# Performance work log

Hardware: AMD Instinct MI355X
Metric: run time of the kernel (lower is better)

## Reference

```python
import jax, jax.numpy as jnp
import numpy as np

VOCAB = 32000; D_MODEL = 768; N_LAYERS = 4
D_STATE = 16; D_CONV = 4; EXPAND = 2
D_INNER = EXPAND * D_MODEL                 # 1536
DT_RANK = (D_MODEL + 15) // 16             # 48
BATCH = 2; SEQ = 1024


def setup_inputs():
    key = jax.random.key(0)
    ks = jax.random.split(key, 10)
    def nrm(k, shape, scale=0.02):
        return (jax.random.normal(k, shape) * scale).astype(jnp.float32)
    inp = {}
    inp['tokens'] = jax.random.randint(ks[0], (BATCH, SEQ), 0, VOCAB)
    inp['embedding'] = nrm(ks[1], (VOCAB, D_MODEL))
    inp['head_bias'] = jnp.zeros((VOCAB,), jnp.float32)
    inp['ln_g'] = jnp.ones((N_LAYERS, D_MODEL), jnp.float32)
    inp['ln_b'] = jnp.zeros((N_LAYERS, D_MODEL), jnp.float32)
    inp['W_in'] = nrm(ks[2], (N_LAYERS, 2 * D_INNER, D_MODEL))
    inp['conv_w'] = nrm(ks[3], (N_LAYERS, D_INNER, 1, D_CONV), 0.1)
    inp['conv_b'] = jnp.zeros((N_LAYERS, D_INNER), jnp.float32)
    inp['W_xproj'] = nrm(ks[4], (N_LAYERS, DT_RANK + 2 * D_STATE, D_INNER))
    inp['W_dt'] = nrm(ks[5], (N_LAYERS, D_INNER, DT_RANK), 0.1)
    inp['b_dt'] = nrm(ks[6], (N_LAYERS, D_INNER), 0.5)
    # S4D-real init: A_n = n for n in 1..d_state
    inp['A_log'] = jnp.broadcast_to(jnp.log(jnp.arange(1, D_STATE + 1, dtype=jnp.float32)), (N_LAYERS, D_INNER, D_STATE)).copy()
    inp['D_ssm'] = jnp.ones((N_LAYERS, D_INNER), jnp.float32)
    inp['W_out'] = nrm(ks[7], (N_LAYERS, D_MODEL, D_INNER))
    inp['norm_g'] = jnp.ones((D_MODEL,), jnp.float32)
    inp['norm_b'] = jnp.zeros((D_MODEL,), jnp.float32)
    return inp


def _ln(x, g, b):
    m = jnp.mean(x, axis=-1, keepdims=True)
    v = jnp.var(x, axis=-1, keepdims=True)
    return (x - m) * jax.lax.rsqrt(v + 1e-5) * g + b


def _mamba(x, W_in, conv_w, conv_b, W_xproj, W_dt, b_dt, A_log, D_ssm, W_out):
    # x: (S, B, D_MODEL)
    xz = jnp.einsum('sbd,ed->sbe', x, W_in)           # (S, B, 2*D_INNER)
    xc, z = jnp.split(xz, 2, axis=-1)
    # depthwise causal conv along sequence
    xt = jnp.transpose(xc, (1, 2, 0))                  # (B, C, S)
    xt = jax.lax.conv_general_dilated(xt, conv_w, (1,), [(D_CONV - 1, 0)],
                                      dimension_numbers=('NCH', 'OIH', 'NCH'),
                                      feature_group_count=D_INNER)
    xt = xt + conv_b[None, :, None]
    xc = jax.nn.silu(jnp.transpose(xt, (2, 0, 1)))     # (S, B, C)
    xdb = jnp.einsum('sbc,ec->sbe', xc, W_xproj)       # (S, B, DT_RANK+2N)
    dt_r = xdb[..., :DT_RANK]
    Bm = xdb[..., DT_RANK:DT_RANK + D_STATE]
    Cm = xdb[..., DT_RANK + D_STATE:]
    dt = jax.nn.softplus(jnp.einsum('sbr,cr->sbc', dt_r, W_dt) + b_dt)
    A = -jnp.exp(A_log)                                # (C, N)

    def step(h, t):
        dt_t, B_t, C_t, x_t = t                        # (B,C),(B,N),(B,N),(B,C)
        dA = jnp.exp(dt_t[..., None] * A)              # (B, C, N)
        h = h * dA + (dt_t * x_t)[..., None] * B_t[:, None, :]
        y = jnp.einsum('bcn,bn->bc', h, C_t)
        return h, y

    h0 = jnp.zeros((x.shape[1], D_INNER, D_STATE), x.dtype)
    _, ys = jax.lax.scan(step, h0, (dt, Bm, Cm, xc))   # ys: (S, B, C)
    y = (ys + D_ssm * xc) * jax.nn.silu(z)
    return jnp.einsum('sbc,dc->sbd', y, W_out)


def reference(tokens, embedding, head_bias, ln_g, ln_b, W_in, conv_w, conv_b, W_xproj, W_dt, b_dt, A_log, D_ssm, W_out, norm_g, norm_b):
    x = embedding[tokens.T]                            # (S, B, D)
    for i in range(N_LAYERS):
        x = x + _mamba(_ln(x, ln_g[i], ln_b[i]), W_in[i], conv_w[i], conv_b[i],
                       W_xproj[i], W_dt[i], b_dt[i], A_log[i], D_ssm[i], W_out[i])
    x = _ln(x, norm_g, norm_b)
    logits = jnp.einsum('sbd,vd->sbv', x, embedding) + head_bias  # tied head
    return jnp.transpose(logits, (1, 0, 2))            # (B, S, VOCAB)
```

## Files before the change

### kernel.cpp

```cpp
#include <hip/hip_runtime.h>
#include <hip/hip_bf16.h>
#include <cstdint>
#include <cstddef>

#define SEQ_LEN 1024
#define NBATCH  2
#define MROWS   2048
#define DMODEL  768
#define DINNER  1536
#define DTRANK  48
#define DSTATE  16
#define NLAYERS 4
#define NVOCAB  32000
#define XPROJ_N 80
#define NCHUNK  16
#define CHUNK   64
#define GROUPS  (NBATCH * DINNER)
#define SCANW   (GROUPS * DSTATE)
#define XSPLIT  8

typedef __attribute__((ext_vector_type(4))) float f32x4;
typedef __attribute__((ext_vector_type(8))) short s16x8;
using bf16 = __hip_bfloat16;

__device__ __forceinline__ float b2f(bf16 v){ return __bfloat162float(v); }
__device__ __forceinline__ bf16  f2b(float v){ return __float2bfloat16(v); }
__device__ __forceinline__ short f2bs(float v){
  return (short)__builtin_bit_cast(unsigned short, __float2bfloat16(v));
}

__device__ __forceinline__ void glds16(const ushort* g, ushort* l) {
  __builtin_amdgcn_global_load_lds(
      (const __attribute__((address_space(1))) void*)g,
      (__attribute__((address_space(3))) void*)l,
      16, 0, 0);
}

#define CVT_E0 6144000
#define CVT_E1 (CVT_E0 + 2359296)
#define CVT_E2 (CVT_E1 + 1179648)
#define CVT_E3 (CVT_E2 + 122880)
#define CVT_E4 (CVT_E3 + 73728)
__global__ __launch_bounds__(256) void k_cvt5(
    const float* __restrict__ s0, const float* __restrict__ s1,
    const float* __restrict__ s2, const float* __restrict__ s3,
    const float* __restrict__ s4,
    ushort* __restrict__ d0, ushort* __restrict__ d1,
    ushort* __restrict__ d2, ushort* __restrict__ d3,
    ushort* __restrict__ d4)
{
  int i = blockIdx.x * 256 + threadIdx.x;
  const float* s; ushort* d; int base;
  if      (i < CVT_E0) { s = s0; d = d0; base = 0; }
  else if (i < CVT_E1) { s = s1; d = d1; base = CVT_E0; }
  else if (i < CVT_E2) { s = s2; d = d2; base = CVT_E1; }
  else if (i < CVT_E3) { s = s3; d = d3; base = CVT_E2; }
  else if (i < CVT_E4) { s = s4; d = d4; base = CVT_E3; }
  else return;
  int li = i - base;
  f32x4 v = *(const f32x4*)(s + (size_t)li * 4);
  ushort4 o;
  o.x = (ushort)f2bs(v[0]); o.y = (ushort)f2bs(v[1]);
  o.z = (ushort)f2bs(v[2]); o.w = (ushort)f2bs(v[3]);
  *(ushort4*)(d + (size_t)li * 4) = o;
}

__global__ __launch_bounds__(256) void k_xsum(const float* __restrict__ p,
    ushort* __restrict__ out, int n4) {
  int i = blockIdx.x * 256 + threadIdx.x;
  if (i >= n4) return;
  f32x4 s = {};
#pragma unroll
  for (int z = 0; z < XSPLIT; z++) {
    f32x4 v = *(const f32x4*)(p + (size_t)z * (MROWS * XPROJ_N) + (size_t)i * 4);
    s[0] += v[0]; s[1] += v[1]; s[2] += v[2]; s[3] += v[3];
  }
  ushort4 o;
  o.x = (ushort)f2bs(s[0]); o.y = (ushort)f2bs(s[1]);
  o.z = (ushort)f2bs(s[2]); o.w = (ushort)f2bs(s[3]);
  *(ushort4*)(out + (size_t)i * 4) = o;
}

__device__ __forceinline__ void ln_rows(const float v0[3], int t,
    const float* __restrict__ g, const float* __restrict__ b,
    bf16* __restrict__ outrow) {
  float s = 0.f, s2 = 0.f;
#pragma unroll
  for (int j = 0; j < 3; j++) { s += v0[j]; s2 += v0[j] * v0[j]; }
#pragma unroll
  for (int o = 32; o >= 1; o >>= 1) { s += __shfl_xor(s, o); s2 += __shfl_xor(s2, o); }
  __shared__ float red[8];
  int wave = t >> 6;
  if ((t & 63) == 0) { red[wave] = s; red[4 + wave] = s2; }
  __syncthreads();
  s  = red[0] + red[1] + red[2] + red[3];
  s2 = red[4] + red[5] + red[6] + red[7];
  float mean = s * (1.f / DMODEL);
  float var  = s2 * (1.f / DMODEL) - mean * mean;
  float rstd = rsqrtf(var + 1e-5f);
#pragma unroll
  for (int j = 0; j < 3; j++) {
    int d = t + j * 256;
    outrow[d] = f2b((v0[j] - mean) * rstd * g[d] + b[d]);
  }
}

__global__ __launch_bounds__(256) void k_ln(const float* __restrict__ x,
    bf16* __restrict__ out, const float* __restrict__ g, const float* __restrict__ b) {
  int m = blockIdx.x;
  const float* row = x + (size_t)m * DMODEL;
  int t = threadIdx.x;
  float v0[3];
#pragma unroll
  for (int j = 0; j < 3; j++) v0[j] = row[t + j * 256];
  ln_rows(v0, t, g, b, out + (size_t)m * DMODEL);
}

__global__ __launch_bounds__(256) void k_embed_ln(const int* __restrict__ tok,
    const float* __restrict__ emb, float* __restrict__ x,
    bf16* __restrict__ out, const float* __restrict__ g, const float* __restrict__ b) {
  int m = blockIdx.x;
  const float* row = emb + (size_t)tok[m] * DMODEL;
  int t = threadIdx.x;
  float v0[3];
#pragma unroll
  for (int j = 0; j < 3; j++) {
    v0[j] = row[t + j * 256];
    x[(size_t)m * DMODEL + t + j * 256] = v0[j];
  }
  ln_rows(v0, t, g, b, out + (size_t)m * DMODEL);
}

template<bool HAS_BIAS, int OMODE>
__global__ __launch_bounds__(256) void k_gemm128(
    const ushort* __restrict__ A, int lda,
    const ushort* __restrict__ B, int ldb,
    void* __restrict__ C, int ldc,
    const float* __restrict__ bias,
    int M, int N, int K)
{
  __shared__ ushort As[2][128 * 32];
  __shared__ ushort Bs[2][128 * 32];
  const int t = threadIdx.x;
  const int lane = t & 63;
  const int wave = t >> 6;
  const int tile_m = blockIdx.x * 128;
  const int tile_n = blockIdx.y * 128;
  const int kper = K / gridDim.z;
  const int kb = blockIdx.z * kper;
  const int ke = kb + kper;
  const int wr = (wave >> 1) * 64;
  const int wc = (wave & 1) * 64;

  f32x4 acc[4][4] = {};

  const int sr = wave * 32 + (lane >> 2);
  const int sc = (lane & 3) * 8;
  const ushort* gA0 = A + (size_t)(tile_m + sr) * lda + sc + kb;
  const ushort* gA1 = gA0 + (size_t)16 * lda;
  const ushort* gB0 = B + (size_t)(tile_n + sr) * ldb + sc + kb;
  const ushort* gB1 = gB0 + (size_t)16 * ldb;

  const int fr = lane & 15;
  const int kk = (lane >> 4) * 8;

  auto stage = [&](int bb) {
    glds16(gA0, &As[bb][wave * 1024]);
    glds16(gA1, &As[bb][wave * 1024 + 512]);
    glds16(gB0, &Bs[bb][wave * 1024]);
    glds16(gB1, &Bs[bb][wave * 1024 + 512]);
    gA0 += 32; gA1 += 32; gB0 += 32; gB1 += 32;
  };

  stage(0);
  int cur = 0;

  for (int k0 = kb; k0 < ke; k0 += 32) {
    if (k0 + 32 < ke) {
      stage(cur ^ 1);
      asm volatile("s_waitcnt vmcnt(4)" ::: "memory");
    } else {
      asm volatile("s_waitcnt vmcnt(0)" ::: "memory");
    }
    __builtin_amdgcn_s_barrier();

    s16x8 a[4], b[4];
#pragma unroll
    for (int m = 0; m < 4; m++)
      a[m] = *(const s16x8*)&As[cur][(wr + m * 16 + fr) * 32 + kk];
#pragma unroll
    for (int n = 0; n < 4; n++)
      b[n] = *(const s16x8*)&Bs[cur][(wc + n * 16 + fr) * 32 + kk];
#pragma unroll
    for (int m = 0; m < 4; m++)
#pragma unroll
      for (int n = 0; n < 4; n++)
        acc[m][n] = __builtin_amdgcn_mfma_f32_16x16x32_bf16(a[m], b[n], acc[m][n], 0, 0, 0);

    __builtin_amdgcn_s_barrier();
    cur ^= 1;
  }

  const int rq = (lane >> 4) * 4;
#pragma unroll
  for (int m = 0; m < 4; m++)
#pragma unroll
    for (int n = 0; n < 4; n++) {
      int colg = tile_n + wc + n * 16 + fr;
      float bv = HAS_BIAS ? bias[colg] : 0.f;
#pragma unroll
      for (int r = 0; r < 4; r++) {
        int rowg = tile_m + wr + m * 16 + rq + r;
        size_t idx = (size_t)rowg * ldc + colg;
        float v = acc[m][n][r] + bv;
        if constexpr (OMODE == 0) ((float*)C)[idx] = v;
        else if constexpr (OMODE == 1) atomicAdd((float*)C + idx, v);
        else ((bf16*)C)[idx] = f2b(v);
      }
    }
}

template<bool HAS_BIAS>
__global__ __launch_bounds__(512) void k_gemm256(
    const ushort* __restrict__ A, int lda,
    const ushort* __restrict__ B, int ldb,
    float* __restrict__ C, int ldc,
    const float* __restrict__ bias,
    int M, int N, int K)
{
  __shared__ ushort As[2][256 * 32];
  __shared__ ushort Bs[2][256 * 32];
  const int t = threadIdx.x;
  const int lane = t & 63;
  const int wave = t >> 6;
  const int tile_m = blockIdx.x * 256;
  const int tile_n = blockIdx.y * 256;
  const int wr = (wave >> 2) * 128;
  const int wc = (wave & 3) * 64;

  f32x4 acc[8][4] = {};

  const int sr = wave * 16 + (lane >> 2);
  const int sc = (lane & 3) * 8;
  const ushort* gA0 = A + (size_t)(tile_m + sr) * lda + sc;
  const ushort* gA1 = A + (size_t)(tile_m + 128 + sr) * lda + sc;
  const ushort* gB0 = B + (size_t)(tile_n + sr) * ldb + sc;
  const ushort* gB1 = B + (size_t)(tile_n + 128 + sr) * ldb + sc;

  const int fr = lane & 15;
  const int kk = (lane >> 4) * 8;

  auto stage = [&](int bb) {
    glds16(gA0, &As[bb][wave * 512]);
    glds16(gA1, &As[bb][4096 + wave * 512]);
    glds16(gB0, &Bs[bb][wave * 512]);
    glds16(gB1, &Bs[bb][4096 + wave * 512]);
    gA0 += 32; gA1 += 32; gB0 += 32; gB1 += 32;
  };

  stage(0);
  int cur = 0;

  for (int k0 = 0; k0 < K; k0 += 32) {
    if (k0 + 32 < K) {
      stage(cur ^ 1);
      asm volatile("s_waitcnt vmcnt(4)" ::: "memory");
    } else {
      asm volatile("s_waitcnt vmcnt(0)" ::: "memory");
    }
    __builtin_amdgcn_s_barrier();

    s16x8 a[8], b[4];
#pragma unroll
    for (int m = 0; m < 8; m++)
      a[m] = *(const s16x8*)&As[cur][(wr + m * 16 + fr) * 32 + kk];
#pragma unroll
    for (int n = 0; n < 4; n++)
      b[n] = *(const s16x8*)&Bs[cur][(wc + n * 16 + fr) * 32 + kk];
#pragma unroll
    for (int m = 0; m < 8; m++)
#pragma unroll
      for (int n = 0; n < 4; n++)
        acc[m][n] = __builtin_amdgcn_mfma_f32_16x16x32_bf16(a[m], b[n], acc[m][n], 0, 0, 0);

    __builtin_amdgcn_s_barrier();
    cur ^= 1;
  }

  const int rq = (lane >> 4) * 4;
#pragma unroll
  for (int m = 0; m < 8; m++)
#pragma unroll
    for (int n = 0; n < 4; n++) {
      int colg = tile_n + wc + n * 16 + fr;
      float bv = HAS_BIAS ? bias[colg] : 0.f;
#pragma unroll
      for (int r = 0; r < 4; r++) {
        int rowg = tile_m + wr + m * 16 + rq + r;
        __builtin_nontemporal_store(acc[m][n][r] + bv, &C[(size_t)rowg * ldc + colg]);
      }
    }
}

template<int MODE>
__global__ __launch_bounds__(256) void k_gemm(
    const ushort* __restrict__ A, int lda,
    const ushort* __restrict__ W, int ldw,
    void* __restrict__ Cout, int ldc,
    int M, int N, int K,
    const float* __restrict__ bias,
    const float* __restrict__ xcp,
    float* __restrict__ dtxp)
{
  __shared__ ushort As[64][40];
  __shared__ ushort Ws[64][40];
  const int tile_m = blockIdx.x * 64;
  const int tile_n = blockIdx.y * 64;
  const int t = threadIdx.x;
  const int lane = t & 63;
  const int wave = t >> 6;
  const int wr = (wave >> 1) * 32;
  const int wc = (wave & 1) * 32;
  f32x4 acc[2][2] = {};

  const int kper = ((K + gridDim.z - 1) / gridDim.z + 31) & ~31;
  const int kb = blockIdx.z * kper;
  int ke = kb + kper; if (ke > K) ke = K;

  const int srow = t >> 2;
  const int scol = (t & 3) * 8;

  for (int k0 = kb; k0 < ke; k0 += 32) {
    {
      int gm = tile_m + srow, gk = k0 + scol;
      s16x8 v = {};
      if (gm < M) {
        if (gk + 8 <= K) v = *(const s16x8*)(A + (size_t)gm * lda + gk);
        else {
#pragma unroll
          for (int j = 0; j < 8; j++) if (gk + j < K) v[j] = (short)A[(size_t)gm * lda + gk + j];
        }
      }
      *(s16x8*)&As[srow][scol] = v;
    }
    {
      int gn = tile_n + srow, gk = k0 + scol;
      s16x8 v = {};
      if (gn < N) {
        if (gk + 8 <= K) v = *(const s16x8*)(W + (size_t)gn * ldw + gk);
        else {
#pragma unroll
          for (int j = 0; j < 8; j++) if (gk + j < K) v[j] = (short)W[(size_t)gn * ldw + gk + j];
        }
      }
      *(s16x8*)&Ws[srow][scol] = v;
    }
    __syncthreads();
    const int kk = (lane >> 4) * 8;
    const int fr = lane & 15;
    s16x8 a0 = *(const s16x8*)&As[wr + fr][kk];
    s16x8 a1 = *(const s16x8*)&As[wr + 16 + fr][kk];
    s16x8 b0 = *(const s16x8*)&Ws[wc + fr][kk];
    s16x8 b1 = *(const s16x8*)&Ws[wc + 16 + fr][kk];
    acc[0][0] = __builtin_amdgcn_mfma_f32_16x16x32_bf16(a0, b0, acc[0][0], 0, 0, 0);
    acc[0][1] = __builtin_amdgcn_mfma_f32_16x16x32_bf16(a0, b1, acc[0][1], 0, 0, 0);
    acc[1][0] = __builtin_amdgcn_mfma_f32_16x16x32_bf16(a1, b0, acc[1][0], 0, 0, 0);
    acc[1][1] = __builtin_amdgcn_mfma_f32_16x16x32_bf16(a1, b1, acc[1][1], 0, 0, 0);
    __syncthreads();
  }

  const int fr = lane & 15;
  const int rq = (lane >> 4) * 4;
#pragma unroll
  for (int i = 0; i < 2; i++)
#pragma unroll
    for (int j = 0; j < 2; j++) {
      int colg = tile_n + wc + j * 16 + fr;
#pragma unroll
      for (int r = 0; r < 4; r++) {
        int rowg = tile_m + wr + i * 16 + rq + r;
        if (rowg < M && colg < N) {
          float v = acc[i][j][r];
          size_t idx = (size_t)rowg * ldc + colg;
          if constexpr (MODE == 0) {
            ((bf16*)Cout)[idx] = f2b(v);
          } else if constexpr (MODE == 2) {
            v += bias[colg];
            float sp = (v > 20.f) ? v : log1pf(__expf(v));
            ((float*)Cout)[idx] = sp;
            dtxp[idx] = sp * xcp[idx];
          } else {
            ((float*)Cout)[(size_t)blockIdx.z * (MROWS * XPROJ_N) + idx] = v;
          }
        }
      }
    }
}

__global__ __launch_bounds__(256) void k_conv(const bf16* __restrict__ xz,
    const float* __restrict__ w, const float* __restrict__ cb,
    float* __restrict__ xc, bf16* __restrict__ xcb) {
  int id = blockIdx.x * 256 + threadIdx.x;
  int m = id / DINNER, c = id - m * DINNER;
  int s = m & (SEQ_LEN - 1);
  float acc = cb[c];
#pragma unroll
  for (int k = 0; k < 4; k++) {
    int sp = s - 3 + k;
    if (sp >= 0) acc += w[c * 4 + k] * b2f(xz[(size_t)(m - 3 + k) * (2 * DINNER) + c]);
  }
  float sil = acc / (1.f + __expf(-acc));
  xc[id] = sil;
  xcb[id] = f2b(sil);
}

__global__ __launch_bounds__(256) void k_scan1(const float* __restrict__ dt,
    const float* __restrict__ dtx, const bf16* __restrict__ xdb,
    const float* __restrict__ A_log, float* __restrict__ aprod,
    float* __restrict__ hend) {
  int gid = blockIdx.x * 256 + threadIdx.x;
  int n  = gid & 15;
  int t2 = gid >> 4;
  int j  = t2 / GROUPS;
  int cb = t2 - j * GROUPS;
  int c  = cb % DINNER;
  int b  = cb / DINNER;
  float Acn = -__expf(A_log[c * DSTATE + n]);
  float h = 0.f, ap = 1.f;
  int mbase = b * SEQ_LEN + j * CHUNK;
#pragma unroll 4
  for (int s = 0; s < CHUNK; s++) {
    int m = mbase + s;
    float dtv = dt[(size_t)m * DINNER + c];
    float dxv = dtx[(size_t)m * DINNER + c];
    float Bv  = b2f(xdb[(size_t)m * XPROJ_N + DTRANK + n]);
    float dA  = __expf(dtv * Acn);
    h = h * dA + dxv * Bv;
    ap *= dA;
  }
  aprod[gid] = ap;
  hend[gid]  = h;
}

__global__ __launch_bounds__(256) void k_scan2(const float* __restrict__ aprod,
    const float* __restrict__ hend, float* __restrict__ hin) {
  int idx = blockIdx.x * 256 + threadIdx.x;
  float h = 0.f;
#pragma unroll
  for (int j = 0; j < NCHUNK; j++) {
    hin[(size_t)j * SCANW + idx] = h;
    h = aprod[(size_t)j * SCANW + idx] * h + hend[(size_t)j * SCANW + idx];
  }
}

__global__ __launch_bounds__(256) void k_scan3(const float* __restrict__ dt,
    const float* __restrict__ dtx, const bf16* __restrict__ xdb,
    const float* __restrict__ A_log, const float* __restrict__ hin,
    float* __restrict__ y) {
  int gid = blockIdx.x * 256 + threadIdx.x;
  int n  = gid & 15;
  int t2 = gid >> 4;
  int j  = t2 / GROUPS;
  int cb = t2 - j * GROUPS;
  int c  = cb % DINNER;
  int b  = cb / DINNER;
  float Acn = -__expf(A_log[c * DSTATE + n]);
  float h = hin[gid];
  int mbase = b * SEQ_LEN + j * CHUNK;
#pragma unroll 2
  for (int s = 0; s < CHUNK; s++) {
    int m = mbase + s;
    float dtv = dt[(size_t)m * DINNER + c];
    float dxv = dtx[(size_t)m * DINNER + c];
    float Bv  = b2f(xdb[(size_t)m * XPROJ_N + DTRANK + n]);
    float Cv  = b2f(xdb[(size_t)m * XPROJ_N + DTRANK + DSTATE + n]);
    float dA  = __expf(dtv * Acn);
    h = h * dA + dxv * Bv;
    float p = h * Cv;
    p += __shfl_xor(p, 8);
    p += __shfl_xor(p, 4);
    p += __shfl_xor(p, 2);
    p += __shfl_xor(p, 1);
    if (n == 0) y[(size_t)m * DINNER + c] = p;
  }
}

__global__ __launch_bounds__(256) void k_ycomb(const float* __restrict__ y,
    const float* __restrict__ xc, const bf16* __restrict__ xz,
    const float* __restrict__ D_ssm, bf16* __restrict__ ybf) {
  int id = blockIdx.x * 256 + threadIdx.x;
  int m = id / DINNER, c = id - m * DINNER;
  float z = b2f(xz[(size_t)m * (2 * DINNER) + DINNER + c]);
  float sil = z / (1.f + __expf(-z));
  float v = (y[id] + D_ssm[c] * xc[id]) * sil;
  ybf[id] = f2b(v);
}

extern "C" void kernel_launch(void* const* d_in, const int* in_sizes, int n_in,
                              void* d_out, int out_size, void* d_ws, size_t ws_size,
                              hipStream_t stream) {
  const int*   tokens    = (const int*)  d_in[0];
  const float* embedding = (const float*)d_in[1];
  const float* head_bias = (const float*)d_in[2];
  const float* ln_g      = (const float*)d_in[3];
  const float* ln_b      = (const float*)d_in[4];
  const float* W_in      = (const float*)d_in[5];
  const float* conv_w    = (const float*)d_in[6];
  const float* conv_b    = (const float*)d_in[7];
  const float* W_xproj   = (const float*)d_in[8];
  const float* W_dt      = (const float*)d_in[9];
  const float* b_dt      = (const float*)d_in[10];
  const float* A_log     = (const float*)d_in[11];
  const float* D_ssm     = (const float*)d_in[12];
  const float* W_out     = (const float*)d_in[13];
  const float* norm_g    = (const float*)d_in[14];
  const float* norm_b    = (const float*)d_in[15];
  float* out = (float*)d_out;

  char* ws = (char*)d_ws;
  size_t off = 0;
  auto alloc = [&](size_t bytes) -> char* {
    char* p = ws + off;
    off = (off + bytes + 255) & ~(size_t)255;
    return p;
  };
  float*  x     = (float*) alloc((size_t)MROWS * DMODEL * 4);
  bf16*   xln   = (bf16*)  alloc((size_t)MROWS * DMODEL * 2);
  bf16*   xz    = (bf16*)  alloc((size_t)MROWS * 2 * DINNER * 2);
  float*  xc    = (float*) alloc((size_t)MROWS * DINNER * 4);
  bf16*   xcb   = (bf16*)  alloc((size_t)MROWS * DINNER * 2);
  bf16*   xdb   = (bf16*)  alloc((size_t)MROWS * XPROJ_N * 2);
  float*  xdbp  = (float*) alloc((size_t)XSPLIT * MROWS * XPROJ_N * 4);
  float*  dtf   = (float*) alloc((size_t)MROWS * DINNER * 4);
  float*  dtx   = (float*) alloc((size_t)MROWS * DINNER * 4);
  float*  yraw  = (float*) alloc((size_t)MROWS * DINNER * 4);
  bf16*   ybf   = (bf16*)  alloc((size_t)MROWS * DINNER * 2);
  float*  aprod = (float*) alloc((size_t)SCANW * NCHUNK * 4);
  float*  hend  = (float*) alloc((size_t)SCANW * NCHUNK * 4);
  float*  hin   = (float*) alloc((size_t)SCANW * NCHUNK * 4);
  ushort* ebf   = (ushort*)alloc((size_t)NVOCAB * DMODEL * 2);
  ushort* winb  = (ushort*)alloc((size_t)NLAYERS * 2 * DINNER * DMODEL * 2);
  ushort* wxpb  = (ushort*)alloc((size_t)NLAYERS * XPROJ_N * DINNER * 2);
  ushort* wdtb  = (ushort*)alloc((size_t)NLAYERS * DINNER * DTRANK * 2);
  ushort* woutb = (ushort*)alloc((size_t)NLAYERS * DMODEL * DINNER * 2);
  (void)ws_size; (void)in_sizes; (void)n_in; (void)out_size;

  k_cvt5<<<(CVT_E4 + 255) / 256, 256, 0, stream>>>(
      embedding, W_in, W_out, W_xproj, W_dt,
      ebf, winb, woutb, wxpb, wdtb);

  k_embed_ln<<<MROWS, 256, 0, stream>>>(tokens, embedding, x, xln, ln_g, ln_b);

  const int XDBN4 = MROWS * XPROJ_N / 4;

  for (int L = 0; L < NLAYERS; L++) {
    if (L > 0)
      k_ln<<<MROWS, 256, 0, stream>>>(x, xln, ln_g + L * DMODEL, ln_b + L * DMODEL);

    k_gemm128<false, 2><<<dim3(MROWS / 128, (2 * DINNER) / 128), 256, 0, stream>>>(
        (const ushort*)xln, DMODEL,
        winb + (size_t)L * 2 * DINNER * DMODEL, DMODEL,
        (void*)xz, 2 * DINNER, nullptr, MROWS, 2 * DINNER, DMODEL);

    k_conv<<<MROWS * DINNER / 256, 256, 0, stream>>>(
        xz, conv_w + (size_t)L * DINNER * 4, conv_b + (size_t)L * DINNER, xc, xcb);

    k_gemm<3><<<dim3(MROWS / 64, 2, XSPLIT), 256, 0, stream>>>(
        (const ushort*)xcb, DINNER,
        wxpb + (size_t)L * XPROJ_N * DINNER, DINNER,
        (void*)xdbp, XPROJ_N, MROWS, XPROJ_N, DINNER,
        nullptr, nullptr, nullptr);
    k_xsum<<<(XDBN4 + 255) / 256, 256, 0, stream>>>(xdbp, (ushort*)xdb, XDBN4);

    k_gemm<2><<<dim3(MROWS / 64, DINNER / 64), 256, 0, stream>>>(
        (const ushort*)xdb, XPROJ_N,
        wdtb + (size_t)L * DINNER * DTRANK, DTRANK,
        (void*)dtf, DINNER, MROWS, DINNER, DTRANK,
        b_dt + (size_t)L * DINNER, xc, dtx);

    const float* Al = A_log + (size_t)L * DINNER * DSTATE;
    k_scan1<<<SCANW * NCHUNK / 256, 256, 0, stream>>>(dtf, dtx, xdb, Al, aprod, hend);
    k_scan2<<<SCANW / 256, 256, 0, stream>>>(aprod, hend, hin);
    k_scan3<<<SCANW * NCHUNK / 256, 256, 0, stream>>>(dtf, dtx, xdb, Al, hin, yraw);

    k_ycomb<<<MROWS * DINNER / 256, 256, 0, stream>>>(
        yraw, xc, xz, D_ssm + (size_t)L * DINNER, ybf);

    k_gemm128<false, 1><<<dim3(MROWS / 128, DMODEL / 128, 4), 256, 0, stream>>>(
        (const ushort*)ybf, DINNER,
        woutb + (size_t)L * DMODEL * DINNER, DINNER,
        (void*)x, DMODEL, nullptr, MROWS, DMODEL, DINNER);
  }

  k_ln<<<MROWS, 256, 0, stream>>>(x, xln, norm_g, norm_b);

  k_gemm256<true><<<dim3(MROWS / 256, NVOCAB / 256), 512, 0, stream>>>(
      (const ushort*)xln, DMODEL,
      ebf, DMODEL,
      out, NVOCAB, head_bias, MROWS, NVOCAB, DMODEL);
}
```

Before: 989.2 us.

## Store SSM intermediates in bf16 and use 8-wave 128x128 GEMM everywhere

Drops the fp32 copy of the conv output and stores dt*x and the scan output y as bf16 instead of fp32, to cut memory traffic in the conv, scan and combine kernels. The 128x128 GEMM moves from 4 to 8 waves, each wave owning a 32x64 sub-tile, for more latency hiding. The 256x256 head GEMM is removed and the vocab projection now uses the 128-tile kernel. This gives up some operand reuse in the large head GEMM and loses some precision in the scan inputs and outputs.

Result: no change. 980.9 us (-0.8%).

```diff
diff --git a/kernel.cpp b/kernel.cpp
--- a/kernel.cpp
+++ b/kernel.cpp
@@ -132,7 +132,7 @@
 }
 
 template<bool HAS_BIAS, int OMODE>
-__global__ __launch_bounds__(256) void k_gemm128(
+__global__ __launch_bounds__(512, 4) void k_gemm128(
     const ushort* __restrict__ A, int lda,
     const ushort* __restrict__ B, int ldb,
     void* __restrict__ C, int ldc,
@@ -149,27 +149,23 @@
   const int kper = K / gridDim.z;
   const int kb = blockIdx.z * kper;
   const int ke = kb + kper;
-  const int wr = (wave >> 1) * 64;
+  const int wr = (wave >> 1) * 32;
   const int wc = (wave & 1) * 64;
 
-  f32x4 acc[4][4] = {};
-
-  const int sr = wave * 32 + (lane >> 2);
+  f32x4 acc[2][4] = {};
+
+  const int sr = wave * 16 + (lane >> 2);
   const int sc = (lane & 3) * 8;
-  const ushort* gA0 = A + (size_t)(tile_m + sr) * lda + sc + kb;
-  const ushort* gA1 = gA0 + (size_t)16 * lda;
-  const ushort* gB0 = B + (size_t)(tile_n + sr) * ldb + sc + kb;
-  const ushort* gB1 = gB0 + (size_t)16 * ldb;
+  const ushort* gA = A + (size_t)(tile_m + sr) * lda + sc + kb;
+  const ushort* gB = B + (size_t)(tile_n + sr) * ldb + sc + kb;
 
   const int fr = lane & 15;
   const int kk = (lane >> 4) * 8;
 
   auto stage = [&](int bb) {
-    glds16(gA0, &As[bb][wave * 1024]);
-    glds16(gA1, &As[bb][wave * 1024 + 512]);
-    glds16(gB0, &Bs[bb][wave * 1024]);
-    glds16(gB1, &Bs[bb][wave * 1024 + 512]);
-    gA0 += 32; gA1 += 32; gB0 += 32; gB1 += 32;
+    glds16(gA, &As[bb][wave * 512]);
+    glds16(gB, &Bs[bb][wave * 512]);
+    gA += 32; gB += 32;
   };
 
   stage(0);
@@ -178,21 +174,21 @@
   for (int k0 = kb; k0 < ke; k0 += 32) {
     if (k0 + 32 < ke) {
       stage(cur ^ 1);
-      asm volatile("s_waitcnt vmcnt(4)" ::: "memory");
+      asm volatile("s_waitcnt vmcnt(2)" ::: "memory");
     } else {
       asm volatile("s_waitcnt vmcnt(0)" ::: "memory");
     }
     __builtin_amdgcn_s_barrier();
 
-    s16x8 a[4], b[4];
-#pragma unroll
-    for (int m = 0; m < 4; m++)
+    s16x8 a[2], b[4];
+#pragma unroll
+    for (int m = 0; m < 2; m++)
       a[m] = *(const s16x8*)&As[cur][(wr + m * 16 + fr) * 32 + kk];
 #pragma unroll
     for (int n = 0; n < 4; n++)
       b[n] = *(const s16x8*)&Bs[cur][(wc + n * 16 + fr) * 32 + kk];
 #pragma unroll
-    for (int m = 0; m < 4; m++)
+    for (int m = 0; m < 2; m++)
 #pragma unroll
       for (int n = 0; n < 4; n++)
         acc[m][n] = __builtin_amdgcn_mfma_f32_16x16x32_bf16(a[m], b[n], acc[m][n], 0, 0, 0);
@@ -203,7 +199,7 @@
 
   const int rq = (lane >> 4) * 4;
 #pragma unroll
-  for (int m = 0; m < 4; m++)
+  for (int m = 0; m < 2; m++)
 #pragma unroll
     for (int n = 0; n < 4; n++) {
       int colg = tile_n + wc + n * 16 + fr;
@@ -220,88 +216,6 @@
     }
 }
 
-template<bool HAS_BIAS>
-__global__ __launch_bounds__(512) void k_gemm256(
-    const ushort* __restrict__ A, int lda,
-    const ushort* __restrict__ B, int ldb,
-    float* __restrict__ C, int ldc,
-    const float* __restrict__ bias,
-    int M, int N, int K)
-{
-  __shared__ ushort As[2][256 * 32];
-  __shared__ ushort Bs[2][256 * 32];
-  const int t = threadIdx.x;
-  const int lane = t & 63;
-  const int wave = t >> 6;
-  const int tile_m = blockIdx.x * 256;
-  const int tile_n = blockIdx.y * 256;
-  const int wr = (wave >> 2) * 128;
-  const int wc = (wave & 3) * 64;
-
-  f32x4 acc[8][4] = {};
-
-  const int sr = wave * 16 + (lane >> 2);
-  const int sc = (lane & 3) * 8;
-  const ushort* gA0 = A + (size_t)(tile_m + sr) * lda + sc;
-  const ushort* gA1 = A + (size_t)(tile_m + 128 + sr) * lda + sc;
-  const ushort* gB0 = B + (size_t)(tile_n + sr) * ldb + sc;
-  const ushort* gB1 = B + (size_t)(tile_n + 128 + sr) * ldb + sc;
-
-  const int fr = lane & 15;
-  const int kk = (lane >> 4) * 8;
-
-  auto stage = [&](int bb) {
-    glds16(gA0, &As[bb][wave * 512]);
-    glds16(gA1, &As[bb][4096 + wave * 512]);
-    glds16(gB0, &Bs[bb][wave * 512]);
-    glds16(gB1, &Bs[bb][4096 + wave * 512]);
-    gA0 += 32; gA1 += 32; gB0 += 32; gB1 += 32;
-  };
-
-  stage(0);
-  int cur = 0;
-
-  for (int k0 = 0; k0 < K; k0 += 32) {
-    if (k0 + 32 < K) {
-      stage(cur ^ 1);
-      asm volatile("s_waitcnt vmcnt(4)" ::: "memory");
-    } else {
-      asm volatile("s_waitcnt vmcnt(0)" ::: "memory");
-    }
-    __builtin_amdgcn_s_barrier();
-
-    s16x8 a[8], b[4];
-#pragma unroll
-    for (int m = 0; m < 8; m++)
-      a[m] = *(const s16x8*)&As[cur][(wr + m * 16 + fr) * 32 + kk];
-#pragma unroll
-    for (int n = 0; n < 4; n++)
-      b[n] = *(const s16x8*)&Bs[cur][(wc + n * 16 + fr) * 32 + kk];
-#pragma unroll
-    for (int m = 0; m < 8; m++)
-#pragma unroll
-      for (int n = 0; n < 4; n++)
-        acc[m][n] = __builtin_amdgcn_mfma_f32_16x16x32_bf16(a[m], b[n], acc[m][n], 0, 0, 0);
-
-    __builtin_amdgcn_s_barrier();
-    cur ^= 1;
-  }
-
-  const int rq = (lane >> 4) * 4;
-#pragma unroll
-  for (int m = 0; m < 8; m++)
-#pragma unroll
-    for (int n = 0; n < 4; n++) {
-      int colg = tile_n + wc + n * 16 + fr;
-      float bv = HAS_BIAS ? bias[colg] : 0.f;
-#pragma unroll
-      for (int r = 0; r < 4; r++) {
-        int rowg = tile_m + wr + m * 16 + rq + r;
-        __builtin_nontemporal_store(acc[m][n][r] + bv, &C[(size_t)rowg * ldc + colg]);
-      }
-    }
-}
-
 template<int MODE>
 __global__ __launch_bounds__(256) void k_gemm(
     const ushort* __restrict__ A, int lda,
@@ -309,8 +223,8 @@
     void* __restrict__ Cout, int ldc,
     int M, int N, int K,
     const float* __restrict__ bias,
-    const float* __restrict__ xcp,
-    float* __restrict__ dtxp)
+    const bf16* __restrict__ xcb,
+    bf16* __restrict__ dtxp)
 {
   __shared__ ushort As[64][40];
   __shared__ ushort Ws[64][40];
@@ -388,7 +302,7 @@
             v += bias[colg];
             float sp = (v > 20.f) ? v : log1pf(__expf(v));
             ((float*)Cout)[idx] = sp;
-            dtxp[idx] = sp * xcp[idx];
+            dtxp[idx] = f2b(sp * b2f(xcb[idx]));
           } else {
             ((float*)Cout)[(size_t)blockIdx.z * (MROWS * XPROJ_N) + idx] = v;
           }
@@ -399,7 +313,7 @@
 
 __global__ __launch_bounds__(256) void k_conv(const bf16* __restrict__ xz,
     const float* __restrict__ w, const float* __restrict__ cb,
-    float* __restrict__ xc, bf16* __restrict__ xcb) {
+    bf16* __restrict__ xcb) {
   int id = blockIdx.x * 256 + threadIdx.x;
   int m = id / DINNER, c = id - m * DINNER;
   int s = m & (SEQ_LEN - 1);
@@ -410,12 +324,11 @@
     if (sp >= 0) acc += w[c * 4 + k] * b2f(xz[(size_t)(m - 3 + k) * (2 * DINNER) + c]);
   }
   float sil = acc / (1.f + __expf(-acc));
-  xc[id] = sil;
   xcb[id] = f2b(sil);
 }
 
 __global__ __launch_bounds__(256) void k_scan1(const float* __restrict__ dt,
-    const float* __restrict__ dtx, const bf16* __restrict__ xdb,
+    const bf16* __restrict__ dtx, const bf16* __restrict__ xdb,
     const float* __restrict__ A_log, float* __restrict__ aprod,
     float* __restrict__ hend) {
   int gid = blockIdx.x * 256 + threadIdx.x;
@@ -432,7 +345,7 @@
   for (int s = 0; s < CHUNK; s++) {
     int m = mbase + s;
     float dtv = dt[(size_t)m * DINNER + c];
-    float dxv = dtx[(size_t)m * DINNER + c];
+    float dxv = b2f(dtx[(size_t)m * DINNER + c]);
     float Bv  = b2f(xdb[(size_t)m * XPROJ_N + DTRANK + n]);
     float dA  = __expf(dtv * Acn);
     h = h * dA + dxv * Bv;
@@ -454,9 +367,9 @@
 }
 
 __global__ __launch_bounds__(256) void k_scan3(const float* __restrict__ dt,
-    const float* __restrict__ dtx, const bf16* __restrict__ xdb,
+    const bf16* __restrict__ dtx, const bf16* __restrict__ xdb,
     const float* __restrict__ A_log, const float* __restrict__ hin,
-    float* __restrict__ y) {
+    bf16* __restrict__ y) {
   int gid = blockIdx.x * 256 + threadIdx.x;
   int n  = gid & 15;
   int t2 = gid >> 4;
@@ -471,7 +384,7 @@
   for (int s = 0; s < CHUNK; s++) {
     int m = mbase + s;
     float dtv = dt[(size_t)m * DINNER + c];
-    float dxv = dtx[(size_t)m * DINNER + c];
+    float dxv = b2f(dtx[(size_t)m * DINNER + c]);
     float Bv  = b2f(xdb[(size_t)m * XPROJ_N + DTRANK + n]);
     float Cv  = b2f(xdb[(size_t)m * XPROJ_N + DTRANK + DSTATE + n]);
     float dA  = __expf(dtv * Acn);
@@ -481,18 +394,18 @@
     p += __shfl_xor(p, 4);
     p += __shfl_xor(p, 2);
     p += __shfl_xor(p, 1);
-    if (n == 0) y[(size_t)m * DINNER + c] = p;
-  }
-}
-
-__global__ __launch_bounds__(256) void k_ycomb(const float* __restrict__ y,
-    const float* __restrict__ xc, const bf16* __restrict__ xz,
+    if (n == 0) y[(size_t)m * DINNER + c] = f2b(p);
+  }
+}
+
+__global__ __launch_bounds__(256) void k_ycomb(const bf16* __restrict__ y,
+    const bf16* __restrict__ xcb, const bf16* __restrict__ xz,
     const float* __restrict__ D_ssm, bf16* __restrict__ ybf) {
   int id = blockIdx.x * 256 + threadIdx.x;
   int m = id / DINNER, c = id - m * DINNER;
   float z = b2f(xz[(size_t)m * (2 * DINNER) + DINNER + c]);
   float sil = z / (1.f + __expf(-z));
-  float v = (y[id] + D_ssm[c] * xc[id]) * sil;
+  float v = (b2f(y[id]) + D_ssm[c] * b2f(xcb[id])) * sil;
   ybf[id] = f2b(v);
 }
 
@@ -527,13 +440,12 @@
   float*  x     = (float*) alloc((size_t)MROWS * DMODEL * 4);
   bf16*   xln   = (bf16*)  alloc((size_t)MROWS * DMODEL * 2);
   bf16*   xz    = (bf16*)  alloc((size_t)MROWS * 2 * DINNER * 2);
-  float*  xc    = (float*) alloc((size_t)MROWS * DINNER * 4);
   bf16*   xcb   = (bf16*)  alloc((size_t)MROWS * DINNER * 2);
   bf16*   xdb   = (bf16*)  alloc((size_t)MROWS * XPROJ_N * 2);
   float*  xdbp  = (float*) alloc((size_t)XSPLIT * MROWS * XPROJ_N * 4);
   float*  dtf   = (float*) alloc((size_t)MROWS * DINNER * 4);
-  float*  dtx   = (float*) alloc((size_t)MROWS * DINNER * 4);
-  float*  yraw  = (float*) alloc((size_t)MROWS * DINNER * 4);
+  bf16*   dtx   = (bf16*)  alloc((size_t)MROWS * DINNER * 2);
+  bf16*   yraw  = (bf16*)  alloc((size_t)MROWS * DINNER * 2);
   bf16*   ybf   = (bf16*)  alloc((size_t)MROWS * DINNER * 2);
   float*  aprod = (float*) alloc((size_t)SCANW * NCHUNK * 4);
   float*  hend  = (float*) alloc((size_t)SCANW * NCHUNK * 4);
@@ -557,13 +469,13 @@
     if (L > 0)
       k_ln<<<MROWS, 256, 0, stream>>>(x, xln, ln_g + L * DMODEL, ln_b + L * DMODEL);
 
-    k_gemm128<false, 2><<<dim3(MROWS / 128, (2 * DINNER) / 128), 256, 0, stream>>>(
+    k_gemm128<false, 2><<<dim3(MROWS / 128, (2 * DINNER) / 128), 512, 0, stream>>>(
         (const ushort*)xln, DMODEL,
         winb + (size_t)L * 2 * DINNER * DMODEL, DMODEL,
         (void*)xz, 2 * DINNER, nullptr, MROWS, 2 * DINNER, DMODEL);
 
     k_conv<<<MROWS * DINNER / 256, 256, 0, stream>>>(
-        xz, conv_w + (size_t)L * DINNER * 4, conv_b + (size_t)L * DINNER, xc, xcb);
+        xz, conv_w + (size_t)L * DINNER * 4, conv_b + (size_t)L * DINNER, xcb);
 
     k_gemm<3><<<dim3(MROWS / 64, 2, XSPLIT), 256, 0, stream>>>(
         (const ushort*)xcb, DINNER,
@@ -576,7 +488,7 @@
         (const ushort*)xdb, XPROJ_N,
         wdtb + (size_t)L * DINNER * DTRANK, DTRANK,
         (void*)dtf, DINNER, MROWS, DINNER, DTRANK,
-        b_dt + (size_t)L * DINNER, xc, dtx);
+        b_dt + (size_t)L * DINNER, xcb, dtx);
 
     const float* Al = A_log + (size_t)L * DINNER * DSTATE;
     k_scan1<<<SCANW * NCHUNK / 256, 256, 0, stream>>>(dtf, dtx, xdb, Al, aprod, hend);
@@ -584,9 +496,9 @@
     k_scan3<<<SCANW * NCHUNK / 256, 256, 0, stream>>>(dtf, dtx, xdb, Al, hin, yraw);
 
     k_ycomb<<<MROWS * DINNER / 256, 256, 0, stream>>>(
-        yraw, xc, xz, D_ssm + (size_t)L * DINNER, ybf);
-
-    k_gemm128<false, 1><<<dim3(MROWS / 128, DMODEL / 128, 4), 256, 0, stream>>>(
+        yraw, xcb, xz, D_ssm + (size_t)L * DINNER, ybf);
+
+    k_gemm128<false, 1><<<dim3(MROWS / 128, DMODEL / 128, 4), 512, 0, stream>>>(
         (const ushort*)ybf, DINNER,
         woutb + (size_t)L * DMODEL * DINNER, DINNER,
         (void*)x, DMODEL, nullptr, MROWS, DMODEL, DINNER);
@@ -594,7 +506,7 @@
 
   k_ln<<<MROWS, 256, 0, stream>>>(x, xln, norm_g, norm_b);
 
-  k_gemm256<true><<<dim3(MROWS / 256, NVOCAB / 256), 512, 0, stream>>>(
+  k_gemm128<true, 0><<<dim3(MROWS / 128, NVOCAB / 128), 512, 0, stream>>>(
       (const ushort*)xln, DMODEL,
       ebf, DMODEL,
       out, NVOCAB, head_bias, MROWS, NVOCAB, DMODEL);
```
